# Kernel optimization log

Hardware: AMD Instinct MI355X
Metric: run time of the kernel (lower is better)

Reference implementation:

```python
import jax, jax.numpy as jnp
import numpy as np

T, N, D, H = 128, 512, 1024, 1024
LN_EPS = 1e-5


def setup_inputs() -> dict:
    key = jax.random.key(0)
    ks = jax.random.split(key, 6)
    x = jax.random.normal(ks[0], (T * N, D), jnp.float32)
    hxs = jax.random.normal(ks[1], (N, 1, H), jnp.float32)
    # binary done-masks (float, mostly 1.0 = keep hidden state, 0.0 = episode reset)
    masks = (jax.random.uniform(ks[2], (T * N, 1)) < 0.95).astype(jnp.float32)
    s = 1.0 / np.sqrt(H)
    # PyTorch GRU packed gates, order (r, z, n): weight_ih_l0 [3H, D], weight_hh_l0 [3H, H]
    W_ih = jax.random.normal(ks[3], (3 * H, D), jnp.float32) * s
    W_hh = jax.random.normal(ks[4], (3 * H, H), jnp.float32) * s
    b_ih = jnp.zeros((3 * H,), jnp.float32)  # module inits biases to 0
    b_hh = jnp.zeros((3 * H,), jnp.float32)
    gamma = jnp.ones((H,), jnp.float32)
    beta = jnp.zeros((H,), jnp.float32)
    return dict(x=x, hxs=hxs, masks=masks, W_ih=W_ih, W_hh=W_hh,
                b_ih=b_ih, b_hh=b_hh, gamma=gamma, beta=beta)


def reference(x, hxs, masks, W_ih, W_hh, b_ih, b_hh, gamma, beta):
    TN = x.shape[0]
    Nn = hxs.shape[0]
    Tt = TN // Nn
    Hd = hxs.shape[-1]
    xs = x.reshape(Tt, Nn, -1)          # [T, N, D]
    m = masks.reshape(Tt, Nn)           # [T, N]
    # Chunk starts per source: t=0 plus every t>=1 where (masks[t] == 1).any().
    # At a chunk start the hidden state is multiplied by masks[t] (broadcast over layers);
    # a scan with a per-step conditional mask-multiply is exactly equivalent to the
    # torch loop over chunks.
    reset = jnp.concatenate([jnp.ones((1,), bool), jnp.any(m[1:] == 1.0, axis=-1)])
    # Batch the input projection across all T*N tokens (one big GEMM): [T, N, 3H]
    xp = jnp.einsum('tnd,gd->tng', xs, W_ih) + b_ih
    h0 = hxs[:, 0, :]                   # recurrent_N == 1 -> [N, H]

    def step(h, inp):
        xp_t, m_t, r_t = inp
        h = jnp.where(r_t, h * m_t[:, None], h)
        hp = h @ W_hh.T + b_hh          # [N, 3H]
        xr, xz, xn = jnp.split(xp_t, 3, axis=-1)
        hr, hz, hn = jnp.split(hp, 3, axis=-1)
        r = jax.nn.sigmoid(xr + hr)
        z = jax.nn.sigmoid(xz + hz)
        n = jnp.tanh(xn + r * hn)
        h_new = (1.0 - z) * n + z * h
        return h_new, h_new

    h_last, outs = jax.lax.scan(step, h0, (xp, m, reset))
    y = outs.reshape(Tt * Nn, Hd)
    # LayerNorm over last dim
    mu = y.mean(-1, keepdims=True)
    var = y.var(-1, keepdims=True)
    y = (y - mu) * jax.lax.rsqrt(var + LN_EPS) * gamma + beta
    return y, h_last[:, None, :]
```

## Files before the change

kernel.cpp:

```cpp
#include <hip/hip_runtime.h>

#define T_STEPS 128
#define N_B     512
#define D_IN    1024
#define H_DIM   1024
#define G_DIM   3072
#define CHUNK   8
#define NCHUNK  16
#define M_CHUNK (CHUNK * N_B)

typedef short          s8v  __attribute__((ext_vector_type(8)));
typedef float          f4v  __attribute__((ext_vector_type(4)));
typedef unsigned short u4v  __attribute__((ext_vector_type(4)));

__device__ __forceinline__ unsigned short f2bf(float f) {
  union { float f; unsigned u; } v; v.f = f;
  unsigned r = v.u + 0x7FFFu + ((v.u >> 16) & 1u);
  return (unsigned short)(r >> 16);
}
__device__ __forceinline__ float bf2f(unsigned short h) {
  union { unsigned u; float f; } v; v.u = ((unsigned)h) << 16;
  return v.f;
}
__device__ __forceinline__ void async16(const void* g, void* l) {
  __builtin_amdgcn_global_load_lds(
      (const __attribute__((address_space(1))) unsigned*)g,
      (__attribute__((address_space(3))) unsigned*)l, 16, 0, 0);
}
__device__ __forceinline__ float sigmoidf_(float x) { return 1.f / (1.f + __expf(-x)); }
__device__ __forceinline__ float tanhf_(float x)    { return 1.f - 2.f / (1.f + __expf(2.f * x)); }

__global__ void cvt_bf16(const float* __restrict__ in, unsigned short* __restrict__ out, long n4) {
  long i = (long)blockIdx.x * blockDim.x + threadIdx.x;
  long stride = (long)gridDim.x * blockDim.x;
  for (; i < n4; i += stride) {
    f4v v = *(const f4v*)(in + i * 4);
    u4v o;
    #pragma unroll
    for (int e = 0; e < 4; ++e) o[e] = f2bf(v[e]);
    *(u4v*)(out + i * 4) = o;
  }
}

__global__ void reset_kernel(const float* __restrict__ masks, int* __restrict__ reset) {
  const int t = blockIdx.x;
  __shared__ int flag;
  if (threadIdx.x == 0) flag = (t == 0) ? 1 : 0;
  __syncthreads();
  if (t > 0 && masks[(size_t)t * N_B + threadIdx.x] == 1.0f) flag = 1;
  __syncthreads();
  if (threadIdx.x == 0) reset[t] = flag;
}

__global__ __launch_bounds__(256) void gemm_xp(const unsigned short* __restrict__ A,
                                               const unsigned short* __restrict__ B,
                                               const float* __restrict__ bias,
                                               unsigned short* __restrict__ C) {
  const int m0 = blockIdx.y * 128, g0 = blockIdx.x * 128;
  const int tid = threadIdx.x, wv = tid >> 6, l = tid & 63;
  const int l15 = l & 15, l4 = l >> 4;
  const int wr = wv >> 1, wc = wv & 1;
  __shared__ unsigned short As[128 * 64], Bs[128 * 64];

  f4v zero4 = {0.f, 0.f, 0.f, 0.f};
  f4v acc[4][4];
  #pragma unroll
  for (int i = 0; i < 4; ++i)
    #pragma unroll
    for (int j = 0; j < 4; ++j) acc[i][j] = zero4;

  const int srow = l >> 3;
  const int selem = (l & 7) * 8;

  for (int kt = 0; kt < 1024; kt += 64) {
    #pragma unroll
    for (int cc = 0; cc < 4; ++cc) {
      int s = wv * 4 + cc;
      int row = s * 8 + srow;
      async16(A + (size_t)(m0 + row) * 1024 + kt + selem, &As[s * 512]);
      async16(B + (size_t)(g0 + row) * 1024 + kt + selem, &Bs[s * 512]);
    }
    __syncthreads();
    #pragma unroll
    for (int ks = 0; ks < 2; ++ks) {
      s8v a[4], b[4];
      #pragma unroll
      for (int i = 0; i < 4; ++i) {
        a[i] = *(const s8v*)&As[(wr * 64 + i * 16 + l15) * 64 + ks * 32 + l4 * 8];
        b[i] = *(const s8v*)&Bs[(wc * 64 + i * 16 + l15) * 64 + ks * 32 + l4 * 8];
      }
      #pragma unroll
      for (int i = 0; i < 4; ++i)
        #pragma unroll
        for (int j = 0; j < 4; ++j)
          acc[i][j] = __builtin_amdgcn_mfma_f32_16x16x32_bf16(a[i], b[j], acc[i][j], 0, 0, 0);
    }
    __syncthreads();
  }
  #pragma unroll
  for (int j = 0; j < 4; ++j) {
    int gcol = g0 + wc * 64 + j * 16 + l15;
    float bv = bias[gcol];
    #pragma unroll
    for (int i = 0; i < 4; ++i) {
      int mrow = m0 + wr * 64 + i * 16 + l4 * 4;
      #pragma unroll
      for (int r = 0; r < 4; ++r)
        C[(size_t)(mrow + r) * G_DIM + gcol] = f2bf(acc[i][j][r] + bv);
    }
  }
}

__global__ __launch_bounds__(256) void gru_step(
    const unsigned short* __restrict__ Whh,
    const unsigned short* __restrict__ xp,
    const float* __restrict__ masks,
    const int* __restrict__ reset,
    const float* __restrict__ bhh,
    const float* __restrict__ hxs,
    const unsigned short* __restrict__ hread,
    unsigned short* __restrict__ hwrite,
    float* __restrict__ y,
    float* __restrict__ hlast,
    int t, int ls) {
  const int bid = blockIdx.x;
  const int jt = bid & 31, nt = bid >> 5;
  const int j0 = jt * 32, n0 = nt * 64;
  const int tid = threadIdx.x, w = tid >> 6, l = tid & 63;
  const int l15 = l & 15, l4 = l >> 4;
  const int wn = w & 1, wj = w >> 1;
  const int l5 = l & 31, lh = l >> 5;

  __shared__ unsigned short Hs[64 * 256];
  __shared__ unsigned short Ws[96 * 256];

  const int rst = reset[t];
  bool zo[2];
  #pragma unroll
  for (int i = 0; i < 2; ++i) {
    float mv = masks[(size_t)t * N_B + n0 + wn * 32 + i * 16 + l15];
    zo[i] = rst && (mv == 0.0f);
  }

  f4v zero4 = {0.f, 0.f, 0.f, 0.f};
  s8v zer8 = {0, 0, 0, 0, 0, 0, 0, 0};
  f4v acc[2][3];
  #pragma unroll
  for (int i = 0; i < 2; ++i)
    #pragma unroll
    for (int g = 0; g < 3; ++g) acc[i][g] = zero4;

  const int swz_rd = (l15 & 7) << 4;

  for (int kt = 0; kt < 1024; kt += 256) {
    #pragma unroll
    for (int q = 0; q < 8; ++q) {
      int rr = q * 8 + w * 2 + lh;
      int kb = (l5 * 16) ^ ((rr & 7) << 4);
      async16(hread + (size_t)(n0 + rr) * H_DIM + kt + (kb >> 1), &Hs[(q * 8 + w * 2) * 256]);
    }
    #pragma unroll
    for (int q = 0; q < 12; ++q) {
      int rr = q * 8 + w * 2 + lh;
      int gate = rr >> 5, jjl = rr & 31;
      int kb = (l5 * 16) ^ ((rr & 7) << 4);
      async16(Whh + ((size_t)gate * H_DIM + j0 + jjl) * H_DIM + kt + (kb >> 1),
              &Ws[(q * 8 + w * 2) * 256]);
    }
    __syncthreads();
    #pragma unroll
    for (int ks = 0; ks < 8; ++ks) {
      const int kbb = (ks * 64 + l4 * 16) ^ swz_rd;
      s8v a[2], b[3];
      #pragma unroll
      for (int i = 0; i < 2; ++i) {
        int rr = wn * 32 + i * 16 + l15;
        a[i] = *(const s8v*)((const char*)Hs + rr * 512 + kbb);
        if (zo[i]) a[i] = zer8;
      }
      #pragma unroll
      for (int g = 0; g < 3; ++g) {
        int rr = g * 32 + wj * 16 + l15;
        b[g] = *(const s8v*)((const char*)Ws + rr * 512 + kbb);
      }
      #pragma unroll
      for (int i = 0; i < 2; ++i)
        #pragma unroll
        for (int g = 0; g < 3; ++g)
          acc[i][g] = __builtin_amdgcn_mfma_f32_16x16x32_bf16(a[i], b[g], acc[i][g], 0, 0, 0);
    }
    __syncthreads();
  }

  const int jj = j0 + wj * 16 + l15;
  const float br = bhh[jj];
  const float bz = bhh[H_DIM + jj];
  const float bn = bhh[2 * H_DIM + jj];
  const float* hsrc = (t == 0) ? hxs : (y + (size_t)(t - 1) * N_B * H_DIM);
  const unsigned short* xpt = xp + (size_t)ls * N_B * G_DIM;

  #pragma unroll
  for (int i = 0; i < 2; ++i) {
    #pragma unroll
    for (int r = 0; r < 4; ++r) {
      const int n = n0 + wn * 32 + i * 16 + l4 * 4 + r;
      const float m = masks[(size_t)t * N_B + n];
      float hprev = hsrc[(size_t)n * H_DIM + jj];
      if (rst && m == 0.0f) hprev = 0.0f;
      const float hr = acc[i][0][r] + br;
      const float hz = acc[i][1][r] + bz;
      const float hn = acc[i][2][r] + bn;
      const size_t xo = (size_t)n * G_DIM + jj;
      const float xr = bf2f(xpt[xo]);
      const float xz = bf2f(xpt[xo + H_DIM]);
      const float xn = bf2f(xpt[xo + 2 * H_DIM]);
      const float rg = sigmoidf_(xr + hr);
      const float zg = sigmoidf_(xz + hz);
      const float ng = tanhf_(xn + rg * hn);
      const float hnew = (1.f - zg) * ng + zg * hprev;
      const size_t gidx = (size_t)n * H_DIM + jj;
      y[(size_t)t * N_B * H_DIM + gidx] = hnew;
      hwrite[gidx] = f2bf(hnew);
      if (t == T_STEPS - 1) hlast[gidx] = hnew;
    }
  }
}

__global__ __launch_bounds__(256) void ln_kernel(float* __restrict__ y,
                                                 const float* __restrict__ gamma,
                                                 const float* __restrict__ beta) {
  const size_t row = blockIdx.x;
  float* p = y + row * (size_t)H_DIM;
  const int tid = threadIdx.x;
  f4v v = *(const f4v*)(p + tid * 4);
  float s = v[0] + v[1] + v[2] + v[3];
  float q = v[0] * v[0] + v[1] * v[1] + v[2] * v[2] + v[3] * v[3];
  #pragma unroll
  for (int off = 32; off > 0; off >>= 1) {
    s += __shfl_down(s, off);
    q += __shfl_down(q, off);
  }
  __shared__ float sb[8];
  const int wid = tid >> 6, lid = tid & 63;
  if (lid == 0) { sb[wid] = s; sb[4 + wid] = q; }
  __syncthreads();
  float S = sb[0] + sb[1] + sb[2] + sb[3];
  float Q = sb[4] + sb[5] + sb[6] + sb[7];
  float mean = S * (1.f / H_DIM);
  float var = Q * (1.f / H_DIM) - mean * mean;
  float inv = rsqrtf(var + 1e-5f);
  f4v g4 = *(const f4v*)(gamma + tid * 4);
  f4v b4 = *(const f4v*)(beta + tid * 4);
  f4v o;
  #pragma unroll
  for (int e = 0; e < 4; ++e) o[e] = (v[e] - mean) * inv * g4[e] + b4[e];
  *(f4v*)(p + tid * 4) = o;
}

extern "C" void kernel_launch(void* const* d_in, const int* in_sizes, int n_in,
                              void* d_out, int out_size, void* d_ws, size_t ws_size,
                              hipStream_t stream) {
  const float* x     = (const float*)d_in[0];
  const float* hxs   = (const float*)d_in[1];
  const float* masks = (const float*)d_in[2];
  const float* W_ih  = (const float*)d_in[3];
  const float* W_hh  = (const float*)d_in[4];
  const float* b_ih  = (const float*)d_in[5];
  const float* b_hh  = (const float*)d_in[6];
  const float* gamma = (const float*)d_in[7];
  const float* beta  = (const float*)d_in[8];
  float* y = (float*)d_out;
  float* hlast = y + (size_t)T_STEPS * N_B * H_DIM;

  char* ws = (char*)d_ws;
  unsigned short* Wih_bf = (unsigned short*)ws;  ws += (size_t)G_DIM * D_IN * 2;
  unsigned short* Whh_bf = (unsigned short*)ws;  ws += (size_t)G_DIM * H_DIM * 2;
  unsigned short* xc_bf  = (unsigned short*)ws;  ws += (size_t)M_CHUNK * D_IN * 2;
  unsigned short* xp_bf  = (unsigned short*)ws;  ws += (size_t)M_CHUNK * G_DIM * 2;
  unsigned short* hbuf   = (unsigned short*)ws;  ws += (size_t)2 * N_B * H_DIM * 2;
  int* reset             = (int*)ws;             ws += 512;

  cvt_bf16<<<1024, 256, 0, stream>>>(W_ih, Wih_bf, (long)G_DIM * D_IN / 4);
  cvt_bf16<<<1024, 256, 0, stream>>>(W_hh, Whh_bf, (long)G_DIM * H_DIM / 4);
  cvt_bf16<<<512, 256, 0, stream>>>(hxs, hbuf, (long)N_B * H_DIM / 4);
  reset_kernel<<<128, 512, 0, stream>>>(masks, reset);

  const size_t NH = (size_t)N_B * H_DIM;
  for (int ck = 0; ck < NCHUNK; ++ck) {
    const float* xck = x + (size_t)ck * M_CHUNK * D_IN;
    cvt_bf16<<<2048, 256, 0, stream>>>(xck, xc_bf, (long)M_CHUNK * D_IN / 4);
    dim3 gg(G_DIM / 128, M_CHUNK / 128);
    gemm_xp<<<gg, 256, 0, stream>>>(xc_bf, Wih_bf, b_ih, xp_bf);

    for (int ls = 0; ls < CHUNK; ++ls) {
      const int t = ck * CHUNK + ls;
      const unsigned short* hread = hbuf + (size_t)(t & 1) * NH;
      unsigned short* hwrite = hbuf + (size_t)((t & 1) ^ 1) * NH;
      gru_step<<<256, 256, 0, stream>>>(Whh_bf, xp_bf, masks, reset, b_hh,
                                        hxs, hread, hwrite, y, hlast, t, ls);
    }
  }

  ln_kernel<<<T_STEPS * N_B, 256, 0, stream>>>(y, gamma, beta);
}
```

Before: 2.753 ms.

## Fuse per-chunk GRU steps into one persistent kernel with group barriers

Replaces the eight per-timestep gru_step launches in each chunk with one persistent kernel that loops over the chunk's timesteps. Blocks are grouped by batch slice, and the 32 blocks of a group sync through an atomic counter barrier, since each block only needs hidden state from its own batch rows. The previous hidden state is kept in registers rather than re-read from y, and the K loop now double-buffers 128-wide LDS tiles so the next tile loads while the current one is computed. This removes launch overhead and the global reload of h, at the cost of spin-wait barriers that assume all 256 blocks are resident at once.

```diff
diff --git a/kernel.cpp b/kernel.cpp
--- a/kernel.cpp
+++ b/kernel.cpp
@@ -111,118 +111,159 @@
   }
 }
 
-__global__ __launch_bounds__(256) void gru_step(
+__global__ __launch_bounds__(256) void rnn_chunk2(
     const unsigned short* __restrict__ Whh,
     const unsigned short* __restrict__ xp,
     const float* __restrict__ masks,
     const int* __restrict__ reset,
     const float* __restrict__ bhh,
     const float* __restrict__ hxs,
-    const unsigned short* __restrict__ hread,
-    unsigned short* __restrict__ hwrite,
-    float* __restrict__ y,
-    float* __restrict__ hlast,
-    int t, int ls) {
+    unsigned short* hbuf,
+    float* y,
+    float* hlast,
+    unsigned* bar,
+    int t0) {
   const int bid = blockIdx.x;
-  const int jt = bid & 31, nt = bid >> 5;
-  const int j0 = jt * 32, n0 = nt * 64;
+  const int g = bid & 7, c = bid >> 3;
+  const int n0 = g * 64, j0 = c * 32;
   const int tid = threadIdx.x, w = tid >> 6, l = tid & 63;
   const int l15 = l & 15, l4 = l >> 4;
   const int wn = w & 1, wj = w >> 1;
-  const int l5 = l & 31, lh = l >> 5;
-
-  __shared__ unsigned short Hs[64 * 256];
-  __shared__ unsigned short Ws[96 * 256];
-
-  const int rst = reset[t];
-  bool zo[2];
-  #pragma unroll
-  for (int i = 0; i < 2; ++i) {
-    float mv = masks[(size_t)t * N_B + n0 + wn * 32 + i * 16 + l15];
-    zo[i] = rst && (mv == 0.0f);
-  }
-
-  f4v zero4 = {0.f, 0.f, 0.f, 0.f};
-  s8v zer8 = {0, 0, 0, 0, 0, 0, 0, 0};
-  f4v acc[2][3];
-  #pragma unroll
-  for (int i = 0; i < 2; ++i)
-    #pragma unroll
-    for (int g = 0; g < 3; ++g) acc[i][g] = zero4;
-
+  const size_t NH = (size_t)N_B * H_DIM;
+
+  __shared__ unsigned short Hs[2][64 * 128];
+  __shared__ unsigned short Ws[2][96 * 128];
+
+  const int lrow4 = l >> 4;
+  const int lcb = (l & 15) * 16;
   const int swz_rd = (l15 & 7) << 4;
-
-  for (int kt = 0; kt < 1024; kt += 256) {
-    #pragma unroll
-    for (int q = 0; q < 8; ++q) {
-      int rr = q * 8 + w * 2 + lh;
-      int kb = (l5 * 16) ^ ((rr & 7) << 4);
-      async16(hread + (size_t)(n0 + rr) * H_DIM + kt + (kb >> 1), &Hs[(q * 8 + w * 2) * 256]);
-    }
-    #pragma unroll
-    for (int q = 0; q < 12; ++q) {
-      int rr = q * 8 + w * 2 + lh;
-      int gate = rr >> 5, jjl = rr & 31;
-      int kb = (l5 * 16) ^ ((rr & 7) << 4);
-      async16(Whh + ((size_t)gate * H_DIM + j0 + jjl) * H_DIM + kt + (kb >> 1),
-              &Ws[(q * 8 + w * 2) * 256]);
-    }
-    __syncthreads();
-    #pragma unroll
-    for (int ks = 0; ks < 8; ++ks) {
-      const int kbb = (ks * 64 + l4 * 16) ^ swz_rd;
-      s8v a[2], b[3];
-      #pragma unroll
-      for (int i = 0; i < 2; ++i) {
-        int rr = wn * 32 + i * 16 + l15;
-        a[i] = *(const s8v*)((const char*)Hs + rr * 512 + kbb);
-        if (zo[i]) a[i] = zer8;
-      }
-      #pragma unroll
-      for (int g = 0; g < 3; ++g) {
-        int rr = g * 32 + wj * 16 + l15;
-        b[g] = *(const s8v*)((const char*)Ws + rr * 512 + kbb);
-      }
-      #pragma unroll
-      for (int i = 0; i < 2; ++i)
-        #pragma unroll
-        for (int g = 0; g < 3; ++g)
-          acc[i][g] = __builtin_amdgcn_mfma_f32_16x16x32_bf16(a[i], b[g], acc[i][g], 0, 0, 0);
-    }
-    __syncthreads();
-  }
 
   const int jj = j0 + wj * 16 + l15;
   const float br = bhh[jj];
   const float bz = bhh[H_DIM + jj];
   const float bn = bhh[2 * H_DIM + jj];
-  const float* hsrc = (t == 0) ? hxs : (y + (size_t)(t - 1) * N_B * H_DIM);
-  const unsigned short* xpt = xp + (size_t)ls * N_B * G_DIM;
-
-  #pragma unroll
-  for (int i = 0; i < 2; ++i) {
-    #pragma unroll
-    for (int r = 0; r < 4; ++r) {
-      const int n = n0 + wn * 32 + i * 16 + l4 * 4 + r;
-      const float m = masks[(size_t)t * N_B + n];
-      float hprev = hsrc[(size_t)n * H_DIM + jj];
-      if (rst && m == 0.0f) hprev = 0.0f;
-      const float hr = acc[i][0][r] + br;
-      const float hz = acc[i][1][r] + bz;
-      const float hn = acc[i][2][r] + bn;
-      const size_t xo = (size_t)n * G_DIM + jj;
-      const float xr = bf2f(xpt[xo]);
-      const float xz = bf2f(xpt[xo + H_DIM]);
-      const float xn = bf2f(xpt[xo + 2 * H_DIM]);
-      const float rg = sigmoidf_(xr + hr);
-      const float zg = sigmoidf_(xz + hz);
-      const float ng = tanhf_(xn + rg * hn);
-      const float hnew = (1.f - zg) * ng + zg * hprev;
-      const size_t gidx = (size_t)n * H_DIM + jj;
-      y[(size_t)t * N_B * H_DIM + gidx] = hnew;
-      hwrite[gidx] = f2bf(hnew);
-      if (t == T_STEPS - 1) hlast[gidx] = hnew;
-    }
+
+  float hreg[2][4];
+  {
+    const float* hsrc = (t0 == 0) ? hxs : (y + (size_t)(t0 - 1) * NH);
+    #pragma unroll
+    for (int i = 0; i < 2; ++i)
+      #pragma unroll
+      for (int r = 0; r < 4; ++r)
+        hreg[i][r] = hsrc[(size_t)(n0 + wn * 32 + i * 16 + l4 * 4 + r) * H_DIM + jj];
+  }
+
+  f4v zero4 = {0.f, 0.f, 0.f, 0.f};
+  s8v zer8 = {0, 0, 0, 0, 0, 0, 0, 0};
+
+  for (int ls = 0; ls < CHUNK; ++ls) {
+    const int t = t0 + ls;
+    const unsigned short* hread = hbuf + (size_t)(t & 1) * NH;
+    unsigned short* hwrite = hbuf + (size_t)((t & 1) ^ 1) * NH;
+    const int rst = reset[t];
+
+    bool zo[2];
+    #pragma unroll
+    for (int i = 0; i < 2; ++i) {
+      float mv = masks[(size_t)t * N_B + n0 + wn * 32 + i * 16 + l15];
+      zo[i] = rst && (mv == 0.0f);
+    }
+
+    f4v acc[2][3];
+    #pragma unroll
+    for (int i = 0; i < 2; ++i)
+      #pragma unroll
+      for (int g3 = 0; g3 < 3; ++g3) acc[i][g3] = zero4;
+
+    auto stageH = [&](int buf, int kt) {
+      #pragma unroll
+      for (int q = 0; q < 4; ++q) {
+        int rb = w * 16 + q * 4;
+        int row = rb + lrow4;
+        int cb = lcb ^ ((row & 7) << 4);
+        async16(hread + (size_t)(n0 + row) * H_DIM + kt * 128 + (cb >> 1),
+                &Hs[buf][rb * 128]);
+      }
+    };
+    auto stageW = [&](int buf, int kt) {
+      #pragma unroll
+      for (int q = 0; q < 6; ++q) {
+        int rb = w * 24 + q * 4;
+        int row = rb + lrow4;
+        int gate = row >> 5, jjl = row & 31;
+        int cb = lcb ^ ((row & 7) << 4);
+        async16(Whh + ((size_t)gate * H_DIM + j0 + jjl) * H_DIM + kt * 128 + (cb >> 1),
+                &Ws[buf][rb * 128]);
+      }
+    };
+
+    stageH(0, 0);
+    stageW(0, 0);
+    __syncthreads();
+
+    for (int kt = 0; kt < 8; ++kt) {
+      const int cur = kt & 1;
+      if (kt < 7) { stageH(cur ^ 1, kt + 1); stageW(cur ^ 1, kt + 1); }
+      const char* hb = (const char*)&Hs[cur][0];
+      const char* wb = (const char*)&Ws[cur][0];
+      #pragma unroll
+      for (int ks = 0; ks < 4; ++ks) {
+        const int kbb = (ks * 64 + l4 * 16) ^ swz_rd;
+        s8v a[2], b[3];
+        #pragma unroll
+        for (int i = 0; i < 2; ++i) {
+          a[i] = *(const s8v*)(hb + (wn * 32 + i * 16 + l15) * 256 + kbb);
+          if (zo[i]) a[i] = zer8;
+        }
+        #pragma unroll
+        for (int g3 = 0; g3 < 3; ++g3)
+          b[g3] = *(const s8v*)(wb + (g3 * 32 + wj * 16 + l15) * 256 + kbb);
+        #pragma unroll
+        for (int i = 0; i < 2; ++i)
+          #pragma unroll
+          for (int g3 = 0; g3 < 3; ++g3)
+            acc[i][g3] = __builtin_amdgcn_mfma_f32_16x16x32_bf16(a[i], b[g3], acc[i][g3], 0, 0, 0);
+      }
+      __syncthreads();
+    }
+
+    const unsigned short* xpt = xp + (size_t)ls * N_B * G_DIM;
+    #pragma unroll
+    for (int i = 0; i < 2; ++i) {
+      #pragma unroll
+      for (int r = 0; r < 4; ++r) {
+        const int n = n0 + wn * 32 + i * 16 + l4 * 4 + r;
+        const float m = masks[(size_t)t * N_B + n];
+        float hprev = hreg[i][r];
+        if (rst && m == 0.0f) hprev = 0.0f;
+        const float hr = acc[i][0][r] + br;
+        const float hz = acc[i][1][r] + bz;
+        const float hn = acc[i][2][r] + bn;
+        const size_t xo = (size_t)n * G_DIM + jj;
+        const float xr = bf2f(xpt[xo]);
+        const float xz = bf2f(xpt[xo + H_DIM]);
+        const float xn = bf2f(xpt[xo + 2 * H_DIM]);
+        const float rg = sigmoidf_(xr + hr);
+        const float zg = sigmoidf_(xz + hz);
+        const float ng = tanhf_(xn + rg * hn);
+        const float hnew = (1.f - zg) * ng + zg * hprev;
+        hreg[i][r] = hnew;
+        const size_t gidx = (size_t)n * H_DIM + jj;
+        y[(size_t)t * NH + gidx] = hnew;
+        hwrite[gidx] = f2bf(hnew);
+        if (t == T_STEPS - 1) hlast[gidx] = hnew;
+      }
+    }
+
+    __syncthreads();
+    if (tid == 0) {
+      __hip_atomic_fetch_add(&bar[g], 1u, __ATOMIC_RELEASE, __HIP_MEMORY_SCOPE_AGENT);
+      const unsigned tgt = 32u * (unsigned)(ls + 1);
+      while (__hip_atomic_load(&bar[g], __ATOMIC_ACQUIRE, __HIP_MEMORY_SCOPE_AGENT) < tgt)
+        __builtin_amdgcn_s_sleep(4);
+    }
+    __syncthreads();
+    __builtin_amdgcn_fence(__ATOMIC_ACQUIRE, "agent");
   }
 }
 
@@ -279,26 +320,22 @@
   unsigned short* xp_bf  = (unsigned short*)ws;  ws += (size_t)M_CHUNK * G_DIM * 2;
   unsigned short* hbuf   = (unsigned short*)ws;  ws += (size_t)2 * N_B * H_DIM * 2;
   int* reset             = (int*)ws;             ws += 512;
-
+  unsigned* bars         = (unsigned*)ws;        ws += NCHUNK * 8 * sizeof(unsigned);
+
+  hipMemsetAsync(bars, 0, NCHUNK * 8 * sizeof(unsigned), stream);
   cvt_bf16<<<1024, 256, 0, stream>>>(W_ih, Wih_bf, (long)G_DIM * D_IN / 4);
   cvt_bf16<<<1024, 256, 0, stream>>>(W_hh, Whh_bf, (long)G_DIM * H_DIM / 4);
   cvt_bf16<<<512, 256, 0, stream>>>(hxs, hbuf, (long)N_B * H_DIM / 4);
   reset_kernel<<<128, 512, 0, stream>>>(masks, reset);
 
-  const size_t NH = (size_t)N_B * H_DIM;
   for (int ck = 0; ck < NCHUNK; ++ck) {
     const float* xck = x + (size_t)ck * M_CHUNK * D_IN;
     cvt_bf16<<<2048, 256, 0, stream>>>(xck, xc_bf, (long)M_CHUNK * D_IN / 4);
     dim3 gg(G_DIM / 128, M_CHUNK / 128);
     gemm_xp<<<gg, 256, 0, stream>>>(xc_bf, Wih_bf, b_ih, xp_bf);
 
-    for (int ls = 0; ls < CHUNK; ++ls) {
-      const int t = ck * CHUNK + ls;
-      const unsigned short* hread = hbuf + (size_t)(t & 1) * NH;
-      unsigned short* hwrite = hbuf + (size_t)((t & 1) ^ 1) * NH;
-      gru_step<<<256, 256, 0, stream>>>(Whh_bf, xp_bf, masks, reset, b_hh,
-                                        hxs, hread, hwrite, y, hlast, t, ls);
-    }
+    rnn_chunk2<<<256, 256, 0, stream>>>(Whh_bf, xp_bf, masks, reset, b_hh,
+                                        hxs, hbuf, y, hlast, bars + ck * 8, ck * CHUNK);
   }
 
   ln_kernel<<<T_STEPS * N_B, 256, 0, stream>>>(y, gamma, beta);
```

Result: slower. 5.184 ms (+88.3%).
